# Kernel tuning notes

Hardware: AMD Instinct MI355X
Metric: run time of the kernel (lower is better)

The kernel has to match this reference:

```python
import jax, jax.numpy as jnp
import numpy as np

K = 3          # kernel_size
OUT = 128      # out_channels
PAD = K // 2   # padding


def setup_inputs() -> dict:
    key = jax.random.key(0)
    k1, k2 = jax.random.split(key)
    x = jax.random.normal(k1, (32, 128, 56, 56), dtype=jnp.float32)
    # FilterStripe weight: [K*K*out_channels, in_channels] (1x1 trailing dims dropped)
    weight = jax.random.normal(k2, (K * K * OUT, 128), dtype=jnp.float32) * 0.05
    return {"x": x, "weight": weight}


def reference(x, weight):
    # The torch forward does: unfold(K, pad=K//2) -> view(b,c,K*K,h,w) -> permute to
    # (b, K*K, c, h, w) -> grouped 1x1 conv with groups=K*K -> sum over the K*K axis.
    # Group g corresponds to kernel tap (kh, kw) with g = kh*K + kw, using filters
    # weight[g*out:(g+1)*out]. Summing over g is exactly a standard KxK convolution
    # with OIHW kernel w[o, c, kh, kw] = weight[(kh*K + kw)*out + o, c].
    in_ch = x.shape[1]
    w = weight.reshape(K, K, OUT, in_ch).transpose(2, 3, 0, 1)  # [out, in, K, K]
    return jax.lax.conv_general_dilated(
        x, w,
        window_strides=(1, 1),
        padding=((PAD, PAD), (PAD, PAD)),
        dimension_numbers=("NCHW", "OIHW", "NCHW"),
    )
```

## Files before the change

### kernel.cpp

```cpp
#include <hip/hip_runtime.h>
#include <hip/hip_bf16.h>

typedef __bf16 bf16x8 __attribute__((ext_vector_type(8)));
typedef float  f32x4  __attribute__((ext_vector_type(4)));

#define HW       3136
#define IMG_W    56
#define IMG_H    56
#define XT_ROW_B 16384
#define XT_IMG_B (58*XT_ROW_B)
#define XT_BYTES ((size_t)32*XT_IMG_B)
#define WGRAN    (9*128*16)
#define WB_BYTES ((size_t)WGRAN*16)
#define PBLK     (32*58)
#define WBLK     (WGRAN/256)
#define CBLK     224

#define AS1 __attribute__((address_space(1)))
#define AS3 __attribute__((address_space(3)))

__global__ __launch_bounds__(256) void prep_kernel(const float* __restrict__ x,
                                                   unsigned char* __restrict__ xt,
                                                   const float* __restrict__ w,
                                                   unsigned char* __restrict__ wb) {
    const int bid = blockIdx.x;
    const int t = threadIdx.x;

    if (bid >= PBLK) {
        int i = (bid - PBLK) * 256 + t;
        if (i >= WGRAN) return;
        const int l15 = i & 15, lq = (i >> 4) & 3, f = (i >> 6) & 1;
        const int c   = (i >> 7) & 3, q32 = (i >> 9) & 3, tap = i >> 11;
        const int oc = q32 * 32 + f * 16 + l15;
        const int ch = c * 32 + lq * 8;
        const float* src = w + (size_t)(tap * 128 + oc) * 128 + ch;
        bf16x8 v;
        #pragma unroll
        for (int j = 0; j < 8; ++j) v[j] = (__bf16)src[j];
        *(bf16x8*)(wb + (size_t)i * 16) = v;
        return;
    }

    __shared__ float ldsF[128 * 65];
    const int swz = (bid & 7) * (PBLK / 8) + (bid >> 3);
    const int n = swz / 58, rt = swz - n * 58;
    unsigned char* row = xt + (size_t)n * XT_IMG_B + (size_t)rt * XT_ROW_B;

    if (rt == 0 || rt == 57) {
        f32x4 z = {0.f, 0.f, 0.f, 0.f};
        #pragma unroll
        for (int i = 0; i < 4; ++i) *(f32x4*)(row + t * 64 + i * 16) = z;
        return;
    }
    const int r = rt - 1;
    const float* xr = x + (size_t)n * 128 * HW + (size_t)r * IMG_W;
    const int wv = t >> 6, lane = t & 63;
    const int wi = min(lane, IMG_W - 1);
    #pragma unroll
    for (int cc = 0; cc < 32; ++cc) {
        int c = cc * 4 + wv;
        float v = xr[(size_t)c * HW + wi];
        ldsF[c * 65 + lane] = (lane < IMG_W) ? v : 0.f;
    }
    __syncthreads();

    const int cl = t >> 2, q = t & 3;
    const bool inb = (cl >= 1) && (cl <= 56);
    #pragma unroll
    for (int g4 = 0; g4 < 4; ++g4) {
        int gi = q * 4 + g4;
        bf16x8 pk;
        #pragma unroll
        for (int j = 0; j < 8; ++j)
            pk[j] = inb ? (__bf16)ldsF[(gi * 8 + j) * 65 + (cl - 1)] : (__bf16)0.0f;
        *(bf16x8*)(row + cl * 256 + ((gi ^ (cl & 7)) * 16)) = pk;
    }
}

template<bool STG>
__device__ __forceinline__ void compute_tile(const unsigned char* xs, const __bf16* wt,
                                             float* on, int oc0, int g7, int tloc,
                                             int obase, int lane,
                                             const unsigned char* tsrc, unsigned char* xsb,
                                             int t, int wv) {
    const int l15 = lane & 15, lq = lane >> 4;
    int vb[7], pr_[7], pc_[7];
    #pragma unroll
    for (int k = 0; k < 7; ++k) {
        int p = (g7 * 7 + k) * 16 + l15;
        int pr = p / 56, pc = p - pr * 56;
        pr_[k] = pr; pc_[k] = pc;
        vb[k] = (4 * tloc + pr + 1) * 16384 + (pc + 1) * 256;
    }
    f32x4 acc[2][7];
    #pragma unroll
    for (int f = 0; f < 2; ++f)
        #pragma unroll
        for (int k = 0; k < 7; ++k) acc[f][k] = (f32x4){0.f, 0.f, 0.f, 0.f};

    #pragma unroll
    for (int tap = 0; tap < 9; ++tap) {
        bf16x8 a[8];
        const __bf16* wn = wt + tap * 16384;
        #pragma unroll
        for (int i = 0; i < 8; ++i)
            a[i] = *(const bf16x8*)(wn + ((i & 3) * 2 + (i >> 2)) * 512);
        if (STG && tap == 1) {
            #pragma unroll
            for (int i = 6; i < 10; ++i)
                #pragma unroll
                for (int j = 0; j < 2; ++j)
                    __builtin_amdgcn_global_load_lds(
                        (const AS1 unsigned int*)(tsrc + i * XT_ROW_B + j * 8192 + t * 16),
                        (AS3 unsigned int*)(xsb + i * 16384 + j * 8192 + wv * 1024),
                        16, 0, 0);
        }
        __builtin_amdgcn_sched_barrier(0);

        const int dh = tap / 3 - 1, dw = tap - (tap / 3) * 3 - 1;
        const int offb = dh * 16384 + dw * 256;
        int sw[7];
        #pragma unroll
        for (int k = 0; k < 7; ++k) sw[k] = (pc_[k] + 1 + dw) & 7;

        __builtin_amdgcn_s_setprio(1);
        #pragma unroll
        for (int c = 0; c < 4; ++c) {
            #pragma unroll
            for (int k = 0; k < 7; ++k) {
                int gi = ((c * 4 + lq) ^ sw[k]) * 16;
                bf16x8 b = *(const bf16x8*)(xs + vb[k] + offb + gi);
                acc[0][k] = __builtin_amdgcn_mfma_f32_16x16x32_bf16(a[c],     b, acc[0][k], 0, 0, 0);
                acc[1][k] = __builtin_amdgcn_mfma_f32_16x16x32_bf16(a[4 + c], b, acc[1][k], 0, 0, 0);
            }
        }
        __builtin_amdgcn_s_setprio(0);
        __builtin_amdgcn_sched_barrier(0);
    }

    #pragma unroll
    for (int f = 0; f < 2; ++f)
        #pragma unroll
        for (int k = 0; k < 7; ++k) {
            int pos = (obase + 4 * tloc + pr_[k]) * 56 + pc_[k];
            int oc  = oc0 + f * 16 + lq * 4;
            #pragma unroll
            for (int rr = 0; rr < 4; ++rr)
                on[(size_t)(oc + rr) * HW + pos] = acc[f][k][rr];
        }
}

__global__ __launch_bounds__(512, 2) void conv_kernel(const unsigned char* __restrict__ xt,
                                                      const unsigned char* __restrict__ wb,
                                                      float* __restrict__ out) {
    __shared__ __align__(16) unsigned char xs[163840];
    const int t = threadIdx.x, lane = t & 63, wv = t >> 6;
    const int b = blockIdx.x;
    const int swz = (b & 7) * 28 + (b >> 3);
    const int img = swz / 7, loc = swz - img * 7;
    const int obase = loc * 8;

    const unsigned char* src = xt + (size_t)img * XT_IMG_B + (size_t)obase * XT_ROW_B;

    #pragma unroll
    for (int i = 0; i < 6; ++i)
        #pragma unroll
        for (int j = 0; j < 2; ++j)
            __builtin_amdgcn_global_load_lds(
                (const AS1 unsigned int*)(src + i * XT_ROW_B + j * 8192 + t * 16),
                (AS3 unsigned int*)(xs + i * 16384 + j * 8192 + wv * 1024),
                16, 0, 0);
    asm volatile("s_waitcnt vmcnt(0)" ::: "memory");
    __builtin_amdgcn_sched_barrier(0);
    __builtin_amdgcn_s_barrier();
    __builtin_amdgcn_sched_barrier(0);

    const int oc0 = (wv & 3) * 32;
    const int g7  = wv >> 2;
    const __bf16* wt = (const __bf16*)(wb + (size_t)(wv & 3) * 8192 + lane * 16);
    float* on = out + (size_t)img * 128 * HW;

    compute_tile<true>(xs, wt, on, oc0, g7, 0, obase, lane, src, xs, t, wv);

    __builtin_amdgcn_sched_barrier(0);
    __builtin_amdgcn_s_barrier();
    __builtin_amdgcn_sched_barrier(0);

    compute_tile<false>(xs, wt, on, oc0, g7, 1, obase, lane, src, xs, t, wv);
}

#define PITCH  272
#define LDSB   (4*64*PITCH)
#define NBLK   896

template<int NPF>
__device__ __forceinline__ void fb_compute(const unsigned char* xs, const float* wf,
                                           float* on, int oc0, int pf0, int r0, int lane) {
    const int l15 = lane & 15, lq = lane >> 4;
    int spb[NPF];
    #pragma unroll
    for (int k = 0; k < NPF; ++k) {
        int p = (pf0 + k) * 16 + l15;
        int r = p / 56, w = p - r * 56;
        spb[k] = ((r + 1) * 64 + (w + 1)) * PITCH + lq * 16;
    }
    f32x4 acc[2][NPF];
    #pragma unroll
    for (int f = 0; f < 2; ++f)
        #pragma unroll
        for (int k = 0; k < NPF; ++k) acc[f][k] = (f32x4){0.f, 0.f, 0.f, 0.f};
    #pragma unroll 3
    for (int tap = 0; tap < 9; ++tap) {
        const int offb  = ((tap / 3) * 64 + (tap % 3) - 65) * PITCH;
        const int wbase = tap * 16384 + oc0 * 128 + l15 * 128 + lq * 8;
        #pragma unroll
        for (int c = 0; c < 4; ++c) {
            bf16x8 a[2];
            #pragma unroll
            for (int f = 0; f < 2; ++f) {
                const float* p = wf + wbase + f * 2048 + c * 32;
                #pragma unroll
                for (int j = 0; j < 8; ++j) a[f][j] = (__bf16)p[j];
            }
            #pragma unroll
            for (int k = 0; k < NPF; ++k) {
                bf16x8 b = *(const bf16x8*)(xs + spb[k] + offb + c * 64);
                #pragma unroll
                for (int f = 0; f < 2; ++f)
                    acc[f][k] = __builtin_amdgcn_mfma_f32_16x16x32_bf16(a[f], b, acc[f][k], 0, 0, 0);
            }
        }
    }
    #pragma unroll
    for (int f = 0; f < 2; ++f)
        #pragma unroll
        for (int k = 0; k < NPF; ++k) {
            int pos = r0 * 56 + (pf0 + k) * 16 + l15;
            int oc  = oc0 + f * 16 + lq * 4;
            #pragma unroll
            for (int rr = 0; rr < 4; ++rr)
                on[(size_t)(oc + rr) * HW + pos] = acc[f][k][rr];
        }
}

__global__ __launch_bounds__(512, 4) void fb_conv_kernel(const float* __restrict__ x,
                                                         const float* __restrict__ wf,
                                                         float* __restrict__ out) {
    __shared__ __align__(16) unsigned char xs[LDSB];
    const int tid = threadIdx.x, lane = tid & 63, wv = tid >> 6;
    const int bid = blockIdx.x;
    const int swz = (bid & 7) * (NBLK / 8) + (bid >> 3);
    const int n = swz / 28, rp = swz - n * 28, r0 = rp * 2;
    if (wv < 4) {
        const float* xn = x + (size_t)n * 128 * HW;
        const int ar = r0 - 1 + wv, wi = lane - 1;
        const bool v = (ar >= 0) & (ar < IMG_H) & (wi >= 0) & (wi < IMG_W);
        const int gc = min(max(ar, 0), IMG_H - 1) * IMG_W + min(max(wi, 0), IMG_W - 1);
        unsigned char* dst = xs + (wv * 64 + lane) * PITCH;
        #pragma unroll
        for (int cg = 0; cg < 16; ++cg) {
            bf16x8 pk;
            #pragma unroll
            for (int j = 0; j < 8; ++j) {
                float f = xn[(size_t)(cg * 8 + j) * HW + gc];
                pk[j] = (__bf16)(v ? f : 0.f);
            }
            *(bf16x8*)(dst + cg * 16) = pk;
        }
    }
    __syncthreads();
    const int oc0 = (wv & 3) * 32;
    float* on = out + (size_t)n * 128 * HW;
    if (wv < 4) fb_compute<4>(xs, wf, on, oc0, 0, r0, lane);
    else        fb_compute<3>(xs, wf, on, oc0, 4, r0, lane);
}

extern "C" void kernel_launch(void* const* d_in, const int* in_sizes, int n_in,
                              void* d_out, int out_size, void* d_ws, size_t ws_size,
                              hipStream_t stream) {
    const float* x = (const float*)d_in[0];
    const float* w = (const float*)d_in[1];
    float* out = (float*)d_out;

    if (ws_size >= XT_BYTES + WB_BYTES) {
        unsigned char* xt = (unsigned char*)d_ws;
        unsigned char* wb = xt + XT_BYTES;
        prep_kernel<<<PBLK + WBLK, 256, 0, stream>>>(x, xt, w, wb);
        conv_kernel<<<CBLK, 512, 0, stream>>>(xt, wb, out);
    } else {
        fb_conv_kernel<<<NBLK, 512, 0, stream>>>(x, w, out);
    }
}
```

Baseline: 54.06 us.

## Retile conv so each wave computes 64 channels over 8 output rows in one pass

Replaces the two-phase compute (4 rows per phase, 32 output channels per wave) with a single pass in which each of the 8 waves covers 64 output channels and 7 pixel groups across all 8 output rows. All 10 input rows are staged into LDS up front instead of in two stages, removing the mid-kernel barrier and staged loads. Weight fragments are double-buffered in registers across the 36 tap/chunk steps. Each LDS B-fragment now feeds 4 MFMAs instead of 2, which halves LDS read traffic per MFMA. In exchange the accumulator count doubles to 112 floats per lane, raising register pressure at 2 blocks/CU, and compute can no longer overlap the loading of the later rows.

```diff
diff --git a/kernel.cpp b/kernel.cpp
--- a/kernel.cpp
+++ b/kernel.cpp
@@ -77,93 +77,20 @@
     }
 }
 
-template<bool STG>
-__device__ __forceinline__ void compute_tile(const unsigned char* xs, const __bf16* wt,
-                                             float* on, int oc0, int g7, int tloc,
-                                             int obase, int lane,
-                                             const unsigned char* tsrc, unsigned char* xsb,
-                                             int t, int wv) {
-    const int l15 = lane & 15, lq = lane >> 4;
-    int vb[7], pr_[7], pc_[7];
-    #pragma unroll
-    for (int k = 0; k < 7; ++k) {
-        int p = (g7 * 7 + k) * 16 + l15;
-        int pr = p / 56, pc = p - pr * 56;
-        pr_[k] = pr; pc_[k] = pc;
-        vb[k] = (4 * tloc + pr + 1) * 16384 + (pc + 1) * 256;
-    }
-    f32x4 acc[2][7];
-    #pragma unroll
-    for (int f = 0; f < 2; ++f)
-        #pragma unroll
-        for (int k = 0; k < 7; ++k) acc[f][k] = (f32x4){0.f, 0.f, 0.f, 0.f};
-
-    #pragma unroll
-    for (int tap = 0; tap < 9; ++tap) {
-        bf16x8 a[8];
-        const __bf16* wn = wt + tap * 16384;
-        #pragma unroll
-        for (int i = 0; i < 8; ++i)
-            a[i] = *(const bf16x8*)(wn + ((i & 3) * 2 + (i >> 2)) * 512);
-        if (STG && tap == 1) {
-            #pragma unroll
-            for (int i = 6; i < 10; ++i)
-                #pragma unroll
-                for (int j = 0; j < 2; ++j)
-                    __builtin_amdgcn_global_load_lds(
-                        (const AS1 unsigned int*)(tsrc + i * XT_ROW_B + j * 8192 + t * 16),
-                        (AS3 unsigned int*)(xsb + i * 16384 + j * 8192 + wv * 1024),
-                        16, 0, 0);
-        }
-        __builtin_amdgcn_sched_barrier(0);
-
-        const int dh = tap / 3 - 1, dw = tap - (tap / 3) * 3 - 1;
-        const int offb = dh * 16384 + dw * 256;
-        int sw[7];
-        #pragma unroll
-        for (int k = 0; k < 7; ++k) sw[k] = (pc_[k] + 1 + dw) & 7;
-
-        __builtin_amdgcn_s_setprio(1);
-        #pragma unroll
-        for (int c = 0; c < 4; ++c) {
-            #pragma unroll
-            for (int k = 0; k < 7; ++k) {
-                int gi = ((c * 4 + lq) ^ sw[k]) * 16;
-                bf16x8 b = *(const bf16x8*)(xs + vb[k] + offb + gi);
-                acc[0][k] = __builtin_amdgcn_mfma_f32_16x16x32_bf16(a[c],     b, acc[0][k], 0, 0, 0);
-                acc[1][k] = __builtin_amdgcn_mfma_f32_16x16x32_bf16(a[4 + c], b, acc[1][k], 0, 0, 0);
-            }
-        }
-        __builtin_amdgcn_s_setprio(0);
-        __builtin_amdgcn_sched_barrier(0);
-    }
-
-    #pragma unroll
-    for (int f = 0; f < 2; ++f)
-        #pragma unroll
-        for (int k = 0; k < 7; ++k) {
-            int pos = (obase + 4 * tloc + pr_[k]) * 56 + pc_[k];
-            int oc  = oc0 + f * 16 + lq * 4;
-            #pragma unroll
-            for (int rr = 0; rr < 4; ++rr)
-                on[(size_t)(oc + rr) * HW + pos] = acc[f][k][rr];
-        }
-}
-
 __global__ __launch_bounds__(512, 2) void conv_kernel(const unsigned char* __restrict__ xt,
                                                       const unsigned char* __restrict__ wb,
                                                       float* __restrict__ out) {
     __shared__ __align__(16) unsigned char xs[163840];
     const int t = threadIdx.x, lane = t & 63, wv = t >> 6;
+    const int l15 = lane & 15, lq = lane >> 4;
     const int b = blockIdx.x;
     const int swz = (b & 7) * 28 + (b >> 3);
     const int img = swz / 7, loc = swz - img * 7;
     const int obase = loc * 8;
 
     const unsigned char* src = xt + (size_t)img * XT_IMG_B + (size_t)obase * XT_ROW_B;
-
-    #pragma unroll
-    for (int i = 0; i < 6; ++i)
+    #pragma unroll
+    for (int i = 0; i < 10; ++i)
         #pragma unroll
         for (int j = 0; j < 2; ++j)
             __builtin_amdgcn_global_load_lds(
@@ -175,18 +102,70 @@
     __builtin_amdgcn_s_barrier();
     __builtin_amdgcn_sched_barrier(0);
 
-    const int oc0 = (wv & 3) * 32;
-    const int g7  = wv >> 2;
-    const __bf16* wt = (const __bf16*)(wb + (size_t)(wv & 3) * 8192 + lane * 16);
+    const int oc0 = (wv & 1) * 64;
+    const int g   = wv >> 1;
+    const unsigned char* wt = wb + (size_t)(wv & 1) * 16384 + lane * 16;
+
+    int base_[7], pr_[7], pc_[7];
+    #pragma unroll
+    for (int k = 0; k < 7; ++k) {
+        int p = (g * 7 + k) * 16 + l15;
+        int pr = p / 56, pc = p - pr * 56;
+        pr_[k] = pr; pc_[k] = pc;
+        base_[k] = (pr + 1) * 16384 + (pc + 1) * 256;
+    }
+
+    f32x4 acc[4][7];
+    #pragma unroll
+    for (int f = 0; f < 4; ++f)
+        #pragma unroll
+        for (int k = 0; k < 7; ++k) acc[f][k] = (f32x4){0.f, 0.f, 0.f, 0.f};
+
+    bf16x8 aB[2][4];
+    #pragma unroll
+    for (int f = 0; f < 4; ++f)
+        aB[0][f] = *(const bf16x8*)(wt + (f >> 1) * 8192 + (f & 1) * 1024);
+
+    #pragma unroll
+    for (int tc = 0; tc < 36; ++tc) {
+        const int tap = tc >> 2, c = tc & 3;
+        if (tc < 35) {
+            const int t2 = (tc + 1) >> 2, c2 = (tc + 1) & 3;
+            #pragma unroll
+            for (int f = 0; f < 4; ++f)
+                aB[(tc + 1) & 1][f] = *(const bf16x8*)(wt + t2 * 32768 + (f >> 1) * 8192
+                                                       + (c2 * 2 + (f & 1)) * 1024);
+        }
+        __builtin_amdgcn_sched_barrier(0);
+
+        const int dh = tap / 3 - 1, dw = tap - (tap / 3) * 3 - 1;
+        const int offb = dh * 16384 + dw * 256;
+        __builtin_amdgcn_s_setprio(1);
+        #pragma unroll
+        for (int k = 0; k < 7; ++k) {
+            int sw = (pc_[k] + 1 + dw) & 7;
+            int gi = ((c * 4 + lq) ^ sw) * 16;
+            bf16x8 bf = *(const bf16x8*)(xs + base_[k] + offb + gi);
+            acc[0][k] = __builtin_amdgcn_mfma_f32_16x16x32_bf16(aB[tc & 1][0], bf, acc[0][k], 0, 0, 0);
+            acc[1][k] = __builtin_amdgcn_mfma_f32_16x16x32_bf16(aB[tc & 1][1], bf, acc[1][k], 0, 0, 0);
+            acc[2][k] = __builtin_amdgcn_mfma_f32_16x16x32_bf16(aB[tc & 1][2], bf, acc[2][k], 0, 0, 0);
+            acc[3][k] = __builtin_amdgcn_mfma_f32_16x16x32_bf16(aB[tc & 1][3], bf, acc[3][k], 0, 0, 0);
+        }
+        __builtin_amdgcn_s_setprio(0);
+        __builtin_amdgcn_sched_barrier(0);
+    }
+
     float* on = out + (size_t)img * 128 * HW;
-
-    compute_tile<true>(xs, wt, on, oc0, g7, 0, obase, lane, src, xs, t, wv);
-
-    __builtin_amdgcn_sched_barrier(0);
-    __builtin_amdgcn_s_barrier();
-    __builtin_amdgcn_sched_barrier(0);
-
-    compute_tile<false>(xs, wt, on, oc0, g7, 1, obase, lane, src, xs, t, wv);
+    #pragma unroll
+    for (int f = 0; f < 4; ++f)
+        #pragma unroll
+        for (int k = 0; k < 7; ++k) {
+            int pos = (obase + pr_[k]) * 56 + pc_[k];
+            int oc  = oc0 + f * 16 + lq * 4;
+            #pragma unroll
+            for (int rr = 0; rr < 4; ++rr)
+                on[(size_t)(oc + rr) * HW + pos] = acc[f][k][rr];
+        }
 }
 
 #define PITCH  272
```

Result: slower. 58.41 us (+8.1%).

## Fuse input transpose and bf16 conversion into the conv kernel's LDS staging

Applied to the files above, without the earlier changes.

Drops the separate prep pass that wrote a padded, swizzled bf16 copy of x to workspace. The conv kernel now reads fp32 x directly, converts each pixel's 8 channels to bf16 and writes them into swizzled LDS. The second tile's rows are staged in two chunks during taps 2 and 4 of the first tile. This saves a full global round trip of the transformed input. In exchange the staging loads are strided fp32 accesses with more instructions per byte, and halo rows are re-read by neighbouring blocks.

```diff
diff --git a/kernel.cpp b/kernel.cpp
--- a/kernel.cpp
+++ b/kernel.cpp
@@ -7,82 +7,49 @@
 #define HW       3136
 #define IMG_W    56
 #define IMG_H    56
-#define XT_ROW_B 16384
-#define XT_IMG_B (58*XT_ROW_B)
-#define XT_BYTES ((size_t)32*XT_IMG_B)
 #define WGRAN    (9*128*16)
 #define WB_BYTES ((size_t)WGRAN*16)
-#define PBLK     (32*58)
-#define WBLK     (WGRAN/256)
 #define CBLK     224
 
 #define AS1 __attribute__((address_space(1)))
 #define AS3 __attribute__((address_space(3)))
 
-__global__ __launch_bounds__(256) void prep_kernel(const float* __restrict__ x,
-                                                   unsigned char* __restrict__ xt,
-                                                   const float* __restrict__ w,
+__global__ __launch_bounds__(256) void wcvt_kernel(const float* __restrict__ w,
                                                    unsigned char* __restrict__ wb) {
-    const int bid = blockIdx.x;
-    const int t = threadIdx.x;
-
-    if (bid >= PBLK) {
-        int i = (bid - PBLK) * 256 + t;
-        if (i >= WGRAN) return;
-        const int l15 = i & 15, lq = (i >> 4) & 3, f = (i >> 6) & 1;
-        const int c   = (i >> 7) & 3, q32 = (i >> 9) & 3, tap = i >> 11;
-        const int oc = q32 * 32 + f * 16 + l15;
-        const int ch = c * 32 + lq * 8;
-        const float* src = w + (size_t)(tap * 128 + oc) * 128 + ch;
-        bf16x8 v;
-        #pragma unroll
-        for (int j = 0; j < 8; ++j) v[j] = (__bf16)src[j];
-        *(bf16x8*)(wb + (size_t)i * 16) = v;
-        return;
-    }
-
-    __shared__ float ldsF[128 * 65];
-    const int swz = (bid & 7) * (PBLK / 8) + (bid >> 3);
-    const int n = swz / 58, rt = swz - n * 58;
-    unsigned char* row = xt + (size_t)n * XT_IMG_B + (size_t)rt * XT_ROW_B;
-
-    if (rt == 0 || rt == 57) {
-        f32x4 z = {0.f, 0.f, 0.f, 0.f};
-        #pragma unroll
-        for (int i = 0; i < 4; ++i) *(f32x4*)(row + t * 64 + i * 16) = z;
-        return;
-    }
-    const int r = rt - 1;
-    const float* xr = x + (size_t)n * 128 * HW + (size_t)r * IMG_W;
-    const int wv = t >> 6, lane = t & 63;
-    const int wi = min(lane, IMG_W - 1);
-    #pragma unroll
-    for (int cc = 0; cc < 32; ++cc) {
-        int c = cc * 4 + wv;
-        float v = xr[(size_t)c * HW + wi];
-        ldsF[c * 65 + lane] = (lane < IMG_W) ? v : 0.f;
-    }
-    __syncthreads();
-
-    const int cl = t >> 2, q = t & 3;
-    const bool inb = (cl >= 1) && (cl <= 56);
-    #pragma unroll
-    for (int g4 = 0; g4 < 4; ++g4) {
-        int gi = q * 4 + g4;
-        bf16x8 pk;
-        #pragma unroll
-        for (int j = 0; j < 8; ++j)
-            pk[j] = inb ? (__bf16)ldsF[(gi * 8 + j) * 65 + (cl - 1)] : (__bf16)0.0f;
-        *(bf16x8*)(row + cl * 256 + ((gi ^ (cl & 7)) * 16)) = pk;
-    }
+    int i = blockIdx.x * 256 + threadIdx.x;
+    if (i >= WGRAN) return;
+    const int l15 = i & 15, lq = (i >> 4) & 3, f = (i >> 6) & 1;
+    const int c   = (i >> 7) & 3, q32 = (i >> 9) & 3, tap = i >> 11;
+    const int oc = q32 * 32 + f * 16 + l15;
+    const int ch = c * 32 + lq * 8;
+    const float* src = w + (size_t)(tap * 128 + oc) * 128 + ch;
+    bf16x8 v;
+    #pragma unroll
+    for (int j = 0; j < 8; ++j) v[j] = (__bf16)src[j];
+    *(bf16x8*)(wb + (size_t)i * 16) = v;
+}
+
+__device__ __forceinline__ void stage_task(unsigned char* xs, const float* __restrict__ xn,
+                                           int obase, int s, int cg, int lane) {
+    const int ar  = obase - 1 + s;
+    const int arc = min(max(ar, 0), IMG_H - 1);
+    const int wcc = min(max(lane - 1, 0), IMG_W - 1);
+    const bool v  = (ar >= 0) & (ar < IMG_H) & (lane >= 1) & (lane <= IMG_W);
+    const float* bp = xn + (size_t)(cg * 8) * HW + arc * IMG_W + wcc;
+    bf16x8 pk;
+    #pragma unroll
+    for (int j = 0; j < 8; ++j) {
+        float f = bp[(size_t)j * HW];
+        pk[j] = (__bf16)(v ? f : 0.f);
+    }
+    *(bf16x8*)(xs + s * 16384 + lane * 256 + ((cg ^ (lane & 7)) * 16)) = pk;
 }
 
 template<bool STG>
-__device__ __forceinline__ void compute_tile(const unsigned char* xs, const __bf16* wt,
+__device__ __forceinline__ void compute_tile(unsigned char* xs, const __bf16* wt,
                                              float* on, int oc0, int g7, int tloc,
                                              int obase, int lane,
-                                             const unsigned char* tsrc, unsigned char* xsb,
-                                             int t, int wv) {
+                                             const float* __restrict__ xn, int wv) {
     const int l15 = lane & 15, lq = lane >> 4;
     int vb[7], pr_[7], pc_[7];
     #pragma unroll
@@ -105,15 +72,19 @@
         #pragma unroll
         for (int i = 0; i < 8; ++i)
             a[i] = *(const bf16x8*)(wn + ((i & 3) * 2 + (i >> 2)) * 512);
-        if (STG && tap == 1) {
-            #pragma unroll
-            for (int i = 6; i < 10; ++i)
-                #pragma unroll
-                for (int j = 0; j < 2; ++j)
-                    __builtin_amdgcn_global_load_lds(
-                        (const AS1 unsigned int*)(tsrc + i * XT_ROW_B + j * 8192 + t * 16),
-                        (AS3 unsigned int*)(xsb + i * 16384 + j * 8192 + wv * 1024),
-                        16, 0, 0);
+        if (STG && tap == 2) {
+            #pragma unroll
+            for (int i = 0; i < 4; ++i) {
+                int tid = 96 + wv + 8 * i;
+                stage_task(xs, xn, obase, 6 + ((tid - 96) >> 4), (tid - 96) & 15, lane);
+            }
+        }
+        if (STG && tap == 4) {
+            #pragma unroll
+            for (int i = 4; i < 8; ++i) {
+                int tid = 96 + wv + 8 * i;
+                stage_task(xs, xn, obase, 6 + ((tid - 96) >> 4), (tid - 96) & 15, lane);
+            }
         }
         __builtin_amdgcn_sched_barrier(0);
 
@@ -150,7 +121,7 @@
         }
 }
 
-__global__ __launch_bounds__(512, 2) void conv_kernel(const unsigned char* __restrict__ xt,
+__global__ __launch_bounds__(512, 2) void conv_kernel(const float* __restrict__ x,
                                                       const unsigned char* __restrict__ wb,
                                                       float* __restrict__ out) {
     __shared__ __align__(16) unsigned char xs[163840];
@@ -160,33 +131,25 @@
     const int img = swz / 7, loc = swz - img * 7;
     const int obase = loc * 8;
 
-    const unsigned char* src = xt + (size_t)img * XT_IMG_B + (size_t)obase * XT_ROW_B;
-
-    #pragma unroll
-    for (int i = 0; i < 6; ++i)
-        #pragma unroll
-        for (int j = 0; j < 2; ++j)
-            __builtin_amdgcn_global_load_lds(
-                (const AS1 unsigned int*)(src + i * XT_ROW_B + j * 8192 + t * 16),
-                (AS3 unsigned int*)(xs + i * 16384 + j * 8192 + wv * 1024),
-                16, 0, 0);
-    asm volatile("s_waitcnt vmcnt(0)" ::: "memory");
-    __builtin_amdgcn_sched_barrier(0);
-    __builtin_amdgcn_s_barrier();
-    __builtin_amdgcn_sched_barrier(0);
+    const float* xn = x + (size_t)img * 128 * HW;
+
+    #pragma unroll 3
+    for (int i = 0; i < 12; ++i) {
+        int tid = wv + 8 * i;
+        stage_task(xs, xn, obase, tid >> 4, tid & 15, lane);
+    }
+    __syncthreads();
 
     const int oc0 = (wv & 3) * 32;
     const int g7  = wv >> 2;
     const __bf16* wt = (const __bf16*)(wb + (size_t)(wv & 3) * 8192 + lane * 16);
     float* on = out + (size_t)img * 128 * HW;
 
-    compute_tile<true>(xs, wt, on, oc0, g7, 0, obase, lane, src, xs, t, wv);
-
-    __builtin_amdgcn_sched_barrier(0);
-    __builtin_amdgcn_s_barrier();
-    __builtin_amdgcn_sched_barrier(0);
-
-    compute_tile<false>(xs, wt, on, oc0, g7, 1, obase, lane, src, xs, t, wv);
+    compute_tile<true>(xs, wt, on, oc0, g7, 0, obase, lane, xn, wv);
+
+    __syncthreads();
+
+    compute_tile<false>(xs, wt, on, oc0, g7, 1, obase, lane, xn, wv);
 }
 
 #define PITCH  272
@@ -282,11 +245,10 @@
     const float* w = (const float*)d_in[1];
     float* out = (float*)d_out;
 
-    if (ws_size >= XT_BYTES + WB_BYTES) {
-        unsigned char* xt = (unsigned char*)d_ws;
-        unsigned char* wb = xt + XT_BYTES;
-        prep_kernel<<<PBLK + WBLK, 256, 0, stream>>>(x, xt, w, wb);
-        conv_kernel<<<CBLK, 512, 0, stream>>>(xt, wb, out);
+    if (ws_size >= WB_BYTES) {
+        unsigned char* wb = (unsigned char*)d_ws;
+        wcvt_kernel<<<(WGRAN + 255) / 256, 256, 0, stream>>>(w, wb);
+        conv_kernel<<<CBLK, 512, 0, stream>>>(x, wb, out);
     } else {
         fb_conv_kernel<<<NBLK, 512, 0, stream>>>(x, w, out);
     }
```

After: 50.33 us. -6.9%, faster.
